# Kernel tuning notes

Hardware: AMD Instinct MI355X
Metric: run time of the kernel (lower is better)

Reference implementation:

```python
import jax, jax.numpy as jnp
import numpy as np

N, F, E, A, H = 50000, 64, 1600000, 8, 16
RECEPTIVE_FIELD = 7


def setup_inputs() -> dict:
    key = jax.random.key(0)
    ks = jax.random.split(key, 12)
    inp = {
        "x": jax.random.normal(ks[0], (N, F), dtype=jnp.float32),
        "edge_index": jax.random.randint(ks[1], (2, E), 0, N, dtype=jnp.int64),
        "w1": jax.random.normal(ks[2], (F, H), dtype=jnp.float32) * 0.1,
        "b1": jax.random.normal(ks[3], (H,), dtype=jnp.float32) * 0.1,
        "w2": jax.random.normal(ks[4], (H, H), dtype=jnp.float32) * 0.1,
        "b2": jax.random.normal(ks[5], (H,), dtype=jnp.float32) * 0.1,
        "w3": jax.random.normal(ks[6], (H, F), dtype=jnp.float32) * 0.1,
        "b3": jax.random.normal(ks[7], (F,), dtype=jnp.float32) * 0.1,
        "fc1_w": jax.random.normal(ks[8], ((1 + RECEPTIVE_FIELD) * F, F), dtype=jnp.float32) * 0.05,
        "fc1_b": jax.random.normal(ks[9], (F,), dtype=jnp.float32) * 0.05,
        "fc2_w": jax.random.normal(ks[10], (F, A), dtype=jnp.float32) * 0.1,
        "fc2_b": jax.random.normal(ks[11], (A,), dtype=jnp.float32) * 0.1,
    }
    return inp


def _mlp(x, w1, b1, w2, b2, w3, b3):
    h = jax.nn.relu(x @ w1 + b1)
    h = jax.nn.relu(h @ w2 + b2)
    return h @ w3 + b3


def _agg_mean(x, src, dst):
    # scatter-mean: mean of source-node features over incoming edges per target
    s = jax.ops.segment_sum(x[src], dst, num_segments=N)          # [N, F]
    cnt = jax.ops.segment_sum(jnp.ones((src.shape[0], 1), x.dtype), dst, num_segments=N)
    return s / jnp.maximum(cnt, 1.0)  # nodes with no in-edges -> 0 (torch mean aggr)


def reference(x, edge_index, w1, b1, w2, b2, w3, b3, fc1_w, fc1_b, fc2_w, fc2_b):
    src, dst = edge_index[0], edge_index[1]
    mlp = lambda t: _mlp(t, w1, b1, w2, b2, w3, b3)
    fields = [mlp(mlp(x))]
    for i in range(RECEPTIVE_FIELD):
        x_ = mlp(x)
        for _ in range(i + 1):
            x_ = _agg_mean(x_, src, dst)
        fields.append(mlp(x_))
    f = jnp.concatenate(fields, axis=1)          # [N, 8*F]
    h = f @ fc1_w + fc1_b                        # [N, F]
    logits = h @ fc2_w + fc2_b                   # [N, A]
    return jax.nn.softmax(logits, axis=-1)       # Categorical probs
```

## Files before the change

### kernel.cpp

```cpp
#include <hip/hip_runtime.h>


#define NB2MAX 400
#define NBLK   256
#define CAP2   32
#define CAPC   48
#define CAPB   6144
#define OVCAP  1024
#define LCAP   6144
#define CAPN   64

__global__ __launch_bounds__(1024) void binfill_k(
    const int* __restrict__ src, const int* __restrict__ dst, int E, int n,
    int* __restrict__ gcur, int* __restrict__ ovbuf,
    int* __restrict__ bins, int* __restrict__ cnts,
    const float* __restrict__ w1, const float* __restrict__ w3,
    const float* __restrict__ b3, const float* __restrict__ fc1w,
    const float* __restrict__ fc1b, const float* __restrict__ fc2w,
    const float* __restrict__ fc2b,
    float* __restrict__ M, float* __restrict__ cvec,
    float* __restrict__ W31, float* __restrict__ c31) {
    __shared__ int lbuf[NB2MAX * CAP2];
    __shared__ int lcnt[NB2MAX];
    __shared__ int lflush[NB2MAX];
    int tid = threadIdx.x;
    int NB = (n + 127) >> 7;

    if ((int)blockIdx.x >= NBLK) {
        float* fl = (float*)lbuf;
        int s = (int)blockIdx.x - NBLK;
        if (s == 0) {
            if (tid < 256) {
                int i = tid >> 4, j = tid & 15;
                float a = 0.f;
                for (int g = 0; g < 64; g++) a += w3[i * 64 + g] * w1[g * 16 + j];
                W31[tid] = a;
            } else if (tid < 272) {
                int j = tid - 256;
                float a = 0.f;
                for (int g = 0; g < 64; g++) a += b3[g] * w1[g * 16 + j];
                c31[j] = a;
            } else if (tid >= 320 && tid < 384) {
                int h = tid - 320;
                float a = 0.f;
                for (int r = 0; r < 512; r++) a += b3[r & 63] * fc1w[r * 64 + h];
                fl[h] = a;
            }
            __syncthreads();
            if (tid < 8) {
                float a = fc2b[tid];
                for (int h = 0; h < 64; h++) a += (fc1b[h] + fl[h]) * fc2w[h * 8 + tid];
                cvec[tid] = a;
            }
        } else {
            int k = s - 1;
            {
                int i = tid >> 6, h = tid & 63;
                float a = 0.f;
                const float* f1 = fc1w + (size_t)(k * 64) * 64 + h;
                for (int g = 0; g < 64; g++) a += w3[i * 64 + g] * f1[g * 64];
                fl[i * 64 + h] = a;
            }
            __syncthreads();
            if (tid < 128) {
                int i = tid >> 3, j = tid & 7;
                float a = 0.f;
                for (int h = 0; h < 64; h++) a += fl[i * 64 + h] * fc2w[h * 8 + j];
                M[k * 128 + i * 8 + j] = a;
            }
        }
        return;
    }

    for (int b = tid; b < NB; b += 1024) { lcnt[b] = 0; lflush[b] = 0; }
    __syncthreads();
    int blk = blockIdx.x;
    int chunk = (E + NBLK - 1) / NBLK;
    int beg = blk * chunk;
    int end = beg + chunk; if (end > E) end = E;
    for (int t0 = beg; t0 < end; t0 += 1024) {
        int e = t0 + tid;
        if (e < end) {
            int d = dst[e], s = src[e];
            if ((unsigned)d < (unsigned)n && (unsigned)s < (unsigned)n) {
                int b = d >> 7;
                int pk = ((d & 127) << 16) | s;
                int pos = atomicAdd(&lcnt[b], 1);
                if (pos < CAP2) lbuf[b * CAP2 + pos] = pk;
                else {
                    int p = atomicAdd(&gcur[b], 1);
                    if (p < OVCAP) ovbuf[b * OVCAP + p] = pk;
                }
            }
        }
        __syncthreads();
        for (int b = tid; b < NB; b += 1024) {
            int cnt = lcnt[b]; if (cnt > CAP2) cnt = CAP2;
            int fl2 = lflush[b];
            size_t cell = ((size_t)b * NBLK + blk) * CAPC;
            int base = 0;
            while (cnt - base >= 16) {
                if (fl2 + 16 <= CAPC) {
                    int* dp = bins + cell + fl2;
                    #pragma unroll
                    for (int q = 0; q < 16; q++) dp[q] = lbuf[b * CAP2 + base + q];
                    fl2 += 16;
                } else {
                    int p = atomicAdd(&gcur[b], 16);
                    for (int q = 0; q < 16; q++)
                        if (p + q < OVCAP) ovbuf[b * OVCAP + p + q] = lbuf[b * CAP2 + base + q];
                }
                base += 16;
            }
            int rem = cnt - base;
            if (base > 0)
                for (int q = 0; q < rem; q++) lbuf[b * CAP2 + q] = lbuf[b * CAP2 + base + q];
            lcnt[b] = rem; lflush[b] = fl2;
        }
        __syncthreads();
    }
    for (int b = tid; b < NB; b += 1024) {
        int cnt = lcnt[b]; if (cnt > CAP2) cnt = CAP2;
        int fl2 = lflush[b];
        size_t cell = ((size_t)b * NBLK + blk) * CAPC;
        if (fl2 + cnt <= CAPC) {
            for (int q = 0; q < cnt; q++) bins[cell + fl2 + q] = lbuf[b * CAP2 + q];
            fl2 += cnt;
        } else {
            int p = atomicAdd(&gcur[b], cnt);
            for (int q = 0; q < cnt; q++)
                if (p + q < OVCAP) ovbuf[b * OVCAP + p + q] = lbuf[b * CAP2 + q];
        }
        cnts[(size_t)blk * NB + b] = fl2;
    }
}

__global__ __launch_bounds__(256) void csr2p_k(
    const int* __restrict__ bins, const int* __restrict__ cnts,
    const int* __restrict__ gcur, const int* __restrict__ ovbuf,
    unsigned short* __restrict__ csrp_s, int2* __restrict__ nd_s,
    int* __restrict__ csr, int2* __restrict__ be, int* __restrict__ lcnt3,
    const float* __restrict__ x, float* __restrict__ z0, float* __restrict__ z1,
    float* __restrict__ logits,
    const float* __restrict__ w1, const float* __restrict__ b1,
    const float* __restrict__ w2, const float* __restrict__ b2,
    const float* __restrict__ W31, const float* __restrict__ c31,
    const float* __restrict__ M0, const float* __restrict__ cvec,
    int n, int NBARG) {
    int tid = threadIdx.x;
    if ((int)blockIdx.x < NBARG) {
        __shared__ int hist[128], pref[128], cur[128], slot[128];
        __shared__ int scnt[NBLK];
        __shared__ int lbuf[LCAP];
        __shared__ int sov;
        __shared__ int ccnt[3], cbase[3];
        int NB = (n + 127) >> 7;
        int b = blockIdx.x;
        if (tid < 128) { hist[tid] = 0; cur[tid] = 0; }
        if (tid < 3) ccnt[tid] = 0;
        scnt[tid] = cnts[(size_t)tid * NB + b];
        if (tid == 0) {
            int g = gcur[b];
            sov = g < 0 ? 0 : (g > OVCAP ? OVCAP : g);
        }
        __syncthreads();
        {
            int c = scnt[tid];
            size_t cell = ((size_t)b * NBLK + tid) * CAPC;
            for (int i = 0; i < c; i++) atomicAdd(&hist[bins[cell + i] >> 16], 1);
        }
        if (tid == 0)
            for (int i = 0; i < sov; i++) atomicAdd(&hist[ovbuf[b * OVCAP + i] >> 16], 1);
        __syncthreads();
        if (tid == 0) {
            int r = 0;
            for (int i = 0; i < 128; i++) { pref[i] = r; r += hist[i]; }
        }
        __syncthreads();
        {
            int c = scnt[tid];
            size_t cell = ((size_t)b * NBLK + tid) * CAPC;
            for (int i = 0; i < c; i++) {
                int pk = bins[cell + i];
                int dl = pk >> 16;
                int pos = pref[dl] + atomicAdd(&cur[dl], 1);
                if (pos < LCAP) lbuf[pos] = pk & 0xffff;
            }
        }
        if (tid == 0) {
            for (int i = 0; i < sov; i++) {
                int pk = ovbuf[b * OVCAP + i];
                int dl = pk >> 16;
                int pos = pref[dl] + atomicAdd(&cur[dl], 1);
                if (pos < LCAP) lbuf[pos] = pk & 0xffff;
            }
        }
        __syncthreads();
        int myc = -1, lpos = 0;
        if (tid < 128) {
            int d = (b << 7) + tid;
            if (d < n) {
                int cnt = hist[tid];
                myc = cnt <= 32 ? 0 : (cnt <= 48 ? 1 : 2);
                lpos = atomicAdd(&ccnt[myc], 1);
            }
        }
        __syncthreads();
        if (tid < 3) cbase[tid] = atomicAdd(&lcnt3[tid], ccnt[tid]);
        __syncthreads();
        if (myc >= 0) {
            int d = (b << 7) + tid;
            int cnt = hist[tid];
            int s = myc * n + cbase[myc] + lpos;
            slot[tid] = s;
            nd_s[s] = make_int2(d, cnt);
            if (cnt > CAPN) {
                int s0 = b * CAPB + pref[tid];
                be[d] = make_int2(s0 + CAPN, s0 + cnt);
                for (int j = CAPN; j < cnt; j++)
                    csr[s0 + j] = lbuf[pref[tid] + j] << 2;
            }
        }
        __syncthreads();
        for (int q = tid; q < 128 * CAPN; q += 256) {
            int dl = q >> 6, j = q & 63;
            int d = (b << 7) + dl;
            if (d >= n) break;
            int cnt = hist[dl];
            int v = (j < cnt) ? lbuf[pref[dl] + j] : n;
            int pos = ((j & 3) << 4) | (j >> 2);
            csrp_s[(size_t)slot[dl] * CAPN + pos] = (unsigned short)v;
        }
        return;
    }
    __shared__ float sw1[1024], sw2[256], sW[256], sM[128];
    __shared__ float sb1[16], sb2[16], sc[16], scv[8];
    for (int i = tid; i < 1024; i += 256) sw1[i] = w1[i];
    sw2[tid] = w2[tid & 255];
    sW[tid & 255] = W31[tid & 255];
    if (tid < 128) sM[tid] = M0[tid];
    if (tid < 16) { sb1[tid] = b1[tid]; sb2[tid] = b2[tid]; sc[tid] = c31[tid]; }
    if (tid < 8) scv[tid] = cvec[tid];
    __syncthreads();
    if ((int)blockIdx.x == NBARG && tid < 16) {
        z0[(size_t)n * 16 + tid] = 0.f;
        z1[(size_t)n * 16 + tid] = 0.f;
    }
    int nid = ((int)blockIdx.x - NBARG) * 256 + tid;
    if (nid >= n) return;
    float t1[16];
    #pragma unroll
    for (int j = 0; j < 16; j++) t1[j] = sb1[j];
    const float4* xp = (const float4*)(x + (size_t)nid * 64);
    #pragma unroll
    for (int q = 0; q < 16; q++) {
        float4 v = xp[q];
        #pragma unroll
        for (int j = 0; j < 16; j++)
            t1[j] += v.x * sw1[(4 * q) * 16 + j] + v.y * sw1[(4 * q + 1) * 16 + j]
                   + v.z * sw1[(4 * q + 2) * 16 + j] + v.w * sw1[(4 * q + 3) * 16 + j];
    }
    #pragma unroll
    for (int j = 0; j < 16; j++) t1[j] = fmaxf(t1[j], 0.f);
    float t2[16];
    #pragma unroll
    for (int j = 0; j < 16; j++) {
        float a = sb2[j];
        #pragma unroll
        for (int i = 0; i < 16; i++) a += t1[i] * sw2[i * 16 + j];
        t2[j] = fmaxf(a, 0.f);
    }
    float z[16];
    #pragma unroll
    for (int j = 0; j < 16; j++) {
        float a = sc[j];
        #pragma unroll
        for (int i = 0; i < 16; i++) a += t2[i] * sW[i * 16 + j];
        z[j] = a;
    }
    float4* zo = (float4*)(z0 + (size_t)nid * 16);
    #pragma unroll
    for (int q = 0; q < 4; q++)
        zo[q] = make_float4(z[4 * q], z[4 * q + 1], z[4 * q + 2], z[4 * q + 3]);
    float h[16], f2[16];
    #pragma unroll
    for (int i = 0; i < 16; i++) h[i] = fmaxf(z[i] + sb1[i], 0.f);
    #pragma unroll
    for (int j = 0; j < 16; j++) {
        float a = sb2[j];
        #pragma unroll
        for (int i = 0; i < 16; i++) a += h[i] * sw2[i * 16 + j];
        f2[j] = fmaxf(a, 0.f);
    }
    float* lp = logits + (size_t)nid * 8;
    #pragma unroll
    for (int j = 0; j < 8; j++) {
        float l = scv[j];
        #pragma unroll
        for (int i = 0; i < 16; i++) l += f2[i] * sM[i * 8 + j];
        lp[j] = l;
    }
}

__global__ __launch_bounds__(256, 4) void hop_k(
    const float* __restrict__ zin, float* __restrict__ zout, float* __restrict__ logits,
    const unsigned short* __restrict__ csrp_s, const int2* __restrict__ nd_s,
    const int2* __restrict__ be, const int* __restrict__ csr,
    const int* __restrict__ lcnt3,
    const float* __restrict__ w2, const float* __restrict__ b1,
    const float* __restrict__ b2, const float* __restrict__ M, int n, int FB) {
    __shared__ float sw2[256], sM[128], sb1[16], sb2[16];
    int tid = threadIdx.x;
    if ((int)blockIdx.x < FB) {
        sw2[tid] = w2[tid];
        if (tid < 128) sM[tid] = M[tid];
        if (tid < 16) { sb1[tid] = b1[tid]; sb2[tid] = b2[tid]; }
        __syncthreads();
        int nid = blockIdx.x * 256 + tid;
        if (nid >= n) return;
        float h[16];
        const float4* zp = (const float4*)(zin + (size_t)nid * 16);
        #pragma unroll
        for (int q = 0; q < 4; q++) {
            float4 v = zp[q];
            h[4 * q] = v.x; h[4 * q + 1] = v.y; h[4 * q + 2] = v.z; h[4 * q + 3] = v.w;
        }
        #pragma unroll
        for (int i = 0; i < 16; i++) h[i] = fmaxf(h[i] + sb1[i], 0.f);
        float t2[16];
        #pragma unroll
        for (int j = 0; j < 16; j++) {
            float a = sb2[j];
            #pragma unroll
            for (int i = 0; i < 16; i++) a += h[i] * sw2[i * 16 + j];
            t2[j] = fmaxf(a, 0.f);
        }
        float* lp = logits + (size_t)nid * 8;
        #pragma unroll
        for (int j = 0; j < 8; j++) {
            float l = 0.f;
            #pragma unroll
            for (int i = 0; i < 16; i++) l += t2[i] * sM[i * 8 + j];
            lp[j] += l;
        }
        return;
    }
    int wave = tid >> 6;
    int lane = tid & 63;
    int quarter = lane >> 4;
    int l16 = lane & 15;
    int t4 = l16 >> 2, ch = l16 & 3;
    int idx = (((int)blockIdx.x - FB) * 4 + wave) * 4 + quarter;
    if (idx >= n) return;
    int ns = lcnt3[0], nm = lcnt3[1];
    int tier; size_t row;
    if (idx < ns)           { tier = 0; row = (size_t)idx; }
    else if (idx < ns + nm) { tier = 1; row = (size_t)n + (idx - ns); }
    else                    { tier = 2; row = 2 * (size_t)n + (idx - ns - nm); }
    int2 nd = nd_s[row];
    int node = nd.x, degi = nd.y;
    const uint4* ip = (const uint4*)(csrp_s + (row << 6));
    uint4 pa = ip[t4 * 2];
    int r0 = pa.x & 0xffff, r1 = pa.x >> 16;
    int r2 = pa.y & 0xffff, r3 = pa.y >> 16;
    int r4 = pa.z & 0xffff, r5 = pa.z >> 16;
    int r6 = pa.w & 0xffff, r7 = pa.w >> 16;
    const float4* z4 = (const float4*)zin;
    float4 v0 = z4[((size_t)r0 << 2) + ch];
    float4 v1 = z4[((size_t)r1 << 2) + ch];
    float4 v2 = z4[((size_t)r2 << 2) + ch];
    float4 v3 = z4[((size_t)r3 << 2) + ch];
    float4 v4 = z4[((size_t)r4 << 2) + ch];
    float4 v5 = z4[((size_t)r5 << 2) + ch];
    float4 v6 = z4[((size_t)r6 << 2) + ch];
    float4 v7 = z4[((size_t)r7 << 2) + ch];
    float ax = ((v0.x + v1.x) + (v2.x + v3.x)) + ((v4.x + v5.x) + (v6.x + v7.x));
    float ay = ((v0.y + v1.y) + (v2.y + v3.y)) + ((v4.y + v5.y) + (v6.y + v7.y));
    float az = ((v0.z + v1.z) + (v2.z + v3.z)) + ((v4.z + v5.z) + (v6.z + v7.z));
    float aw = ((v0.w + v1.w) + (v2.w + v3.w)) + ((v4.w + v5.w) + (v6.w + v7.w));
    if (tier >= 1) {
        uint4 pb = ip[t4 * 2 + 1];
        int r8 = pb.x & 0xffff, r9 = pb.x >> 16;
        int rA = pb.y & 0xffff, rB = pb.y >> 16;
        float4 v8 = z4[((size_t)r8 << 2) + ch];
        float4 v9 = z4[((size_t)r9 << 2) + ch];
        float4 vA = z4[((size_t)rA << 2) + ch];
        float4 vB = z4[((size_t)rB << 2) + ch];
        ax += (v8.x + v9.x) + (vA.x + vB.x);
        ay += (v8.y + v9.y) + (vA.y + vB.y);
        az += (v8.z + v9.z) + (vA.z + vB.z);
        aw += (v8.w + v9.w) + (vA.w + vB.w);
        if (tier == 2) {
            int rC = pb.z & 0xffff, rD = pb.z >> 16;
            int rE = pb.w & 0xffff, rF = pb.w >> 16;
            float4 vC = z4[((size_t)rC << 2) + ch];
            float4 vD = z4[((size_t)rD << 2) + ch];
            float4 vE = z4[((size_t)rE << 2) + ch];
            float4 vF = z4[((size_t)rF << 2) + ch];
            ax += (vC.x + vD.x) + (vE.x + vF.x);
            ay += (vC.y + vD.y) + (vE.y + vF.y);
            az += (vC.z + vD.z) + (vE.z + vF.z);
            aw += (vC.w + vD.w) + (vE.w + vF.w);
            if (degi > CAPN) {
                int2 r = be[node];
                for (int q = r.x + t4; q < r.y; q += 4) {
                    float4 v = z4[(size_t)csr[q] + ch];
                    ax += v.x; ay += v.y; az += v.z; aw += v.w;
                }
            }
        }
    }
    #pragma unroll
    for (int off = 8; off >= 4; off >>= 1) {
        ax += __shfl_down(ax, off, 16);
        ay += __shfl_down(ay, off, 16);
        az += __shfl_down(az, off, 16);
        aw += __shfl_down(aw, off, 16);
    }
    if (l16 < 4) {
        float inv = 1.f / (float)(degi > 0 ? degi : 1);
        ((float4*)(zout + (size_t)node * 16))[l16] =
            make_float4(ax * inv, ay * inv, az * inv, aw * inv);
    }
}

__global__ __launch_bounds__(256) void fieldsoft_k(
    const float* __restrict__ z, float* __restrict__ logits,
    const float* __restrict__ w2, const float* __restrict__ b1,
    const float* __restrict__ b2, const float* __restrict__ M, int n) {
    __shared__ float sw2[256], sM[128], sb1[16], sb2[16];
    int tid = threadIdx.x;
    sw2[tid] = w2[tid];
    if (tid < 128) sM[tid] = M[tid];
    if (tid < 16) { sb1[tid] = b1[tid]; sb2[tid] = b2[tid]; }
    __syncthreads();
    int nid = blockIdx.x * 256 + tid;
    if (nid >= n) return;
    float h[16];
    const float4* zp = (const float4*)(z + (size_t)nid * 16);
    #pragma unroll
    for (int q = 0; q < 4; q++) {
        float4 v = zp[q];
        h[4 * q] = v.x; h[4 * q + 1] = v.y; h[4 * q + 2] = v.z; h[4 * q + 3] = v.w;
    }
    #pragma unroll
    for (int i = 0; i < 16; i++) h[i] = fmaxf(h[i] + sb1[i], 0.f);
    float t2[16];
    #pragma unroll
    for (int j = 0; j < 16; j++) {
        float a = sb2[j];
        #pragma unroll
        for (int i = 0; i < 16; i++) a += h[i] * sw2[i * 16 + j];
        t2[j] = fmaxf(a, 0.f);
    }
    float4* lp4 = (float4*)(logits + (size_t)nid * 8);
    float4 l0 = lp4[0], l1 = lp4[1];
    float v[8] = {l0.x, l0.y, l0.z, l0.w, l1.x, l1.y, l1.z, l1.w};
    #pragma unroll
    for (int j = 0; j < 8; j++) {
        float l = 0.f;
        #pragma unroll
        for (int i = 0; i < 16; i++) l += t2[i] * sM[i * 8 + j];
        v[j] += l;
    }
    float m = v[0];
    #pragma unroll
    for (int j = 1; j < 8; j++) m = fmaxf(m, v[j]);
    float s = 0.f;
    #pragma unroll
    for (int j = 0; j < 8; j++) { v[j] = expf(v[j] - m); s += v[j]; }
    float inv = 1.f / s;
    lp4[0] = make_float4(v[0] * inv, v[1] * inv, v[2] * inv, v[3] * inv);
    lp4[1] = make_float4(v[4] * inv, v[5] * inv, v[6] * inv, v[7] * inv);
}

extern "C" void kernel_launch(void* const* d_in, const int* in_sizes, int n_in,
                              void* d_out, int out_size, void* d_ws, size_t ws_size,
                              hipStream_t stream) {
    const float* x    = (const float*)d_in[0];
    const int*   ei   = (const int*)d_in[1];
    const float* w1   = (const float*)d_in[2];
    const float* b1   = (const float*)d_in[3];
    const float* w2   = (const float*)d_in[4];
    const float* b2   = (const float*)d_in[5];
    const float* w3   = (const float*)d_in[6];
    const float* b3   = (const float*)d_in[7];
    const float* fc1w = (const float*)d_in[8];
    const float* fc1b = (const float*)d_in[9];
    const float* fc2w = (const float*)d_in[10];
    const float* fc2b = (const float*)d_in[11];
    float* out = (float*)d_out;

    int n = in_sizes[0] / 64;
    int E = in_sizes[1] / 2;
    int NB = (n + 127) >> 7;
    const int* src = ei;
    const int* dst = ei + E;

    char* ws = (char*)d_ws;
    auto carve = [&](size_t bytes) {
        char* p = ws;
        ws += (bytes + 255) & ~((size_t)255);
        return p;
    };
    int*   gcur    = (int*)carve((size_t)NB * 4);
    int*   lcnt3   = (int*)carve(16);
    int*   ovbuf   = (int*)carve((size_t)NB * OVCAP * 4);
    int*   binsbuf = (int*)carve((size_t)NB * NBLK * CAPC * 4);
    int*   cnts    = (int*)carve((size_t)NBLK * NB * 4);
    unsigned short* csrp_s = (unsigned short*)carve((size_t)3 * n * CAPN * 2);
    int2*  nd_s    = (int2*)carve((size_t)3 * n * 8);
    int*   csr     = (int*)carve((size_t)NB * CAPB * 4);
    int2*  be      = (int2*)carve((size_t)n * 8);
    float* buf0    = (float*)carve((size_t)(n + 1) * 16 * 4);
    float* buf1    = (float*)carve((size_t)(n + 1) * 16 * 4);
    float* M       = (float*)carve(1024 * 4);
    float* cvec    = (float*)carve(8 * 4);
    float* W31     = (float*)carve(256 * 4);
    float* c31     = (float*)carve(16 * 4);

    size_t gpad = ((size_t)NB * 4 + 255) & ~((size_t)255);
    hipMemsetAsync(gcur, 0, gpad + 16, stream);
    binfill_k<<<NBLK + 9, 1024, 0, stream>>>(src, dst, E, n, gcur, ovbuf, binsbuf, cnts,
                                             w1, w3, b3, fc1w, fc1b, fc2w, fc2b,
                                             M, cvec, W31, c31);

    int FB = (n + 255) / 256;
    int AB = (n + 15) / 16;
    csr2p_k<<<NB + FB, 256, 0, stream>>>(binsbuf, cnts, gcur, ovbuf,
                                         csrp_s, nd_s, csr, be, lcnt3,
                                         x, buf0, buf1, out, w1, b1, w2, b2,
                                         W31, c31, M, cvec, n, NB);

    float* cur = buf0;
    float* nxt = buf1;
    hop_k<<<AB, 256, 0, stream>>>(cur, nxt, out, csrp_s, nd_s, be, csr, lcnt3,
                                  w2, b1, b2, M, n, 0);
    { float* t = cur; cur = nxt; nxt = t; }
    for (int k = 1; k <= 6; k++) {
        hop_k<<<FB + AB, 256, 0, stream>>>(cur, nxt, out, csrp_s, nd_s, be, csr,
                                           lcnt3, w2, b1, b2, M + k * 128, n, FB);
        float* t = cur; cur = nxt; nxt = t;
    }
    fieldsoft_k<<<FB, 256, 0, stream>>>(cur, out, w2, b1, b2, M + 7 * 128, n);
}
```

Before: 260.8 us.

## Store hop features in fp16 and split CSR build from projection kernel

```diff
diff --git a/kernel.cpp b/kernel.cpp
--- a/kernel.cpp
+++ b/kernel.cpp
@@ -1,4 +1,5 @@
 #include <hip/hip_runtime.h>
+#include <hip/hip_fp16.h>
 
 
 #define NB2MAX 400
@@ -135,106 +136,115 @@
     }
 }
 
-__global__ __launch_bounds__(256) void csr2p_k(
+__global__ __launch_bounds__(256) void csr2_k(
     const int* __restrict__ bins, const int* __restrict__ cnts,
     const int* __restrict__ gcur, const int* __restrict__ ovbuf,
     unsigned short* __restrict__ csrp_s, int2* __restrict__ nd_s,
     int* __restrict__ csr, int2* __restrict__ be, int* __restrict__ lcnt3,
-    const float* __restrict__ x, float* __restrict__ z0, float* __restrict__ z1,
+    int n) {
+    __shared__ int hist[128], pref[128], cur[128], slot[128];
+    __shared__ int scnt[NBLK];
+    __shared__ int lbuf[LCAP];
+    __shared__ int sov;
+    __shared__ int ccnt[3], cbase[3];
+    int tid = threadIdx.x;
+    int NB = (n + 127) >> 7;
+    int b = blockIdx.x;
+    if (tid < 128) { hist[tid] = 0; cur[tid] = 0; }
+    if (tid < 3) ccnt[tid] = 0;
+    scnt[tid] = cnts[(size_t)tid * NB + b];
+    if (tid == 0) {
+        int g = gcur[b];
+        sov = g < 0 ? 0 : (g > OVCAP ? OVCAP : g);
+    }
+    __syncthreads();
+    {
+        int c = scnt[tid];
+        size_t cell = ((size_t)b * NBLK + tid) * CAPC;
+        for (int i = 0; i < c; i++) atomicAdd(&hist[bins[cell + i] >> 16], 1);
+    }
+    if (tid == 0)
+        for (int i = 0; i < sov; i++) atomicAdd(&hist[ovbuf[b * OVCAP + i] >> 16], 1);
+    __syncthreads();
+    if (tid == 0) {
+        int r = 0;
+        for (int i = 0; i < 128; i++) { pref[i] = r; r += hist[i]; }
+    }
+    __syncthreads();
+    {
+        int c = scnt[tid];
+        size_t cell = ((size_t)b * NBLK + tid) * CAPC;
+        for (int i = 0; i < c; i++) {
+            int pk = bins[cell + i];
+            int dl = pk >> 16;
+            int pos = pref[dl] + atomicAdd(&cur[dl], 1);
+            if (pos < LCAP) lbuf[pos] = pk & 0xffff;
+        }
+    }
+    if (tid == 0) {
+        for (int i = 0; i < sov; i++) {
+            int pk = ovbuf[b * OVCAP + i];
+            int dl = pk >> 16;
+            int pos = pref[dl] + atomicAdd(&cur[dl], 1);
+            if (pos < LCAP) lbuf[pos] = pk & 0xffff;
+        }
+    }
+    __syncthreads();
+    int myc = -1, lpos = 0;
+    if (tid < 128) {
+        int d = (b << 7) + tid;
+        if (d < n) {
+            int cnt = hist[tid];
+            myc = cnt <= 32 ? 0 : (cnt <= 48 ? 1 : 2);
+            lpos = atomicAdd(&ccnt[myc], 1);
+        }
+    }
+    __syncthreads();
+    if (tid < 3) cbase[tid] = atomicAdd(&lcnt3[tid], ccnt[tid]);
+    __syncthreads();
+    if (myc >= 0) {
+        int d = (b << 7) + tid;
+        int cnt = hist[tid];
+        int s = myc * n + cbase[myc] + lpos;
+        slot[tid] = s;
+        nd_s[s] = make_int2(d, cnt);
+        if (cnt > CAPN) {
+            int s0 = b * CAPB + pref[tid];
+            be[d] = make_int2(s0 + CAPN, s0 + cnt);
+            for (int j = CAPN; j < cnt; j++)
+                csr[s0 + j] = lbuf[pref[tid] + j] << 2;
+        }
+    }
+    __syncthreads();
+    for (int q = tid; q < 128 * CAPN; q += 256) {
+        int dl = q >> 6, j = q & 63;
+        int d = (b << 7) + dl;
+        if (d >= n) break;
+        int cnt = hist[dl];
+        int v = (j < cnt) ? lbuf[pref[dl] + j] : n;
+        int pos = ((j & 3) << 4) | (j >> 2);
+        csrp_s[(size_t)slot[dl] * CAPN + pos] = (unsigned short)v;
+    }
+}
+
+__device__ __forceinline__ void acc_row(uint2 u, float& ax, float& ay,
+                                        float& az, float& aw) {
+    __half2 p = *reinterpret_cast<const __half2*>(&u.x);
+    __half2 q = *reinterpret_cast<const __half2*>(&u.y);
+    float2 f = __half22float2(p), g = __half22float2(q);
+    ax += f.x; ay += f.y; az += g.x; aw += g.y;
+}
+
+__global__ __launch_bounds__(256) void proj_k(
+    const float* __restrict__ x, __half* __restrict__ z0, __half* __restrict__ z1,
     float* __restrict__ logits,
     const float* __restrict__ w1, const float* __restrict__ b1,
     const float* __restrict__ w2, const float* __restrict__ b2,
     const float* __restrict__ W31, const float* __restrict__ c31,
-    const float* __restrict__ M0, const float* __restrict__ cvec,
-    int n, int NBARG) {
-    int tid = threadIdx.x;
-    if ((int)blockIdx.x < NBARG) {
-        __shared__ int hist[128], pref[128], cur[128], slot[128];
-        __shared__ int scnt[NBLK];
-        __shared__ int lbuf[LCAP];
-        __shared__ int sov;
-        __shared__ int ccnt[3], cbase[3];
-        int NB = (n + 127) >> 7;
-        int b = blockIdx.x;
-        if (tid < 128) { hist[tid] = 0; cur[tid] = 0; }
-        if (tid < 3) ccnt[tid] = 0;
-        scnt[tid] = cnts[(size_t)tid * NB + b];
-        if (tid == 0) {
-            int g = gcur[b];
-            sov = g < 0 ? 0 : (g > OVCAP ? OVCAP : g);
-        }
-        __syncthreads();
-        {
-            int c = scnt[tid];
-            size_t cell = ((size_t)b * NBLK + tid) * CAPC;
-            for (int i = 0; i < c; i++) atomicAdd(&hist[bins[cell + i] >> 16], 1);
-        }
-        if (tid == 0)
-            for (int i = 0; i < sov; i++) atomicAdd(&hist[ovbuf[b * OVCAP + i] >> 16], 1);
-        __syncthreads();
-        if (tid == 0) {
-            int r = 0;
-            for (int i = 0; i < 128; i++) { pref[i] = r; r += hist[i]; }
-        }
-        __syncthreads();
-        {
-            int c = scnt[tid];
-            size_t cell = ((size_t)b * NBLK + tid) * CAPC;
-            for (int i = 0; i < c; i++) {
-                int pk = bins[cell + i];
-                int dl = pk >> 16;
-                int pos = pref[dl] + atomicAdd(&cur[dl], 1);
-                if (pos < LCAP) lbuf[pos] = pk & 0xffff;
-            }
-        }
-        if (tid == 0) {
-            for (int i = 0; i < sov; i++) {
-                int pk = ovbuf[b * OVCAP + i];
-                int dl = pk >> 16;
-                int pos = pref[dl] + atomicAdd(&cur[dl], 1);
-                if (pos < LCAP) lbuf[pos] = pk & 0xffff;
-            }
-        }
-        __syncthreads();
-        int myc = -1, lpos = 0;
-        if (tid < 128) {
-            int d = (b << 7) + tid;
-            if (d < n) {
-                int cnt = hist[tid];
-                myc = cnt <= 32 ? 0 : (cnt <= 48 ? 1 : 2);
-                lpos = atomicAdd(&ccnt[myc], 1);
-            }
-        }
-        __syncthreads();
-        if (tid < 3) cbase[tid] = atomicAdd(&lcnt3[tid], ccnt[tid]);
-        __syncthreads();
-        if (myc >= 0) {
-            int d = (b << 7) + tid;
-            int cnt = hist[tid];
-            int s = myc * n + cbase[myc] + lpos;
-            slot[tid] = s;
-            nd_s[s] = make_int2(d, cnt);
-            if (cnt > CAPN) {
-                int s0 = b * CAPB + pref[tid];
-                be[d] = make_int2(s0 + CAPN, s0 + cnt);
-                for (int j = CAPN; j < cnt; j++)
-                    csr[s0 + j] = lbuf[pref[tid] + j] << 2;
-            }
-        }
-        __syncthreads();
-        for (int q = tid; q < 128 * CAPN; q += 256) {
-            int dl = q >> 6, j = q & 63;
-            int d = (b << 7) + dl;
-            if (d >= n) break;
-            int cnt = hist[dl];
-            int v = (j < cnt) ? lbuf[pref[dl] + j] : n;
-            int pos = ((j & 3) << 4) | (j >> 2);
-            csrp_s[(size_t)slot[dl] * CAPN + pos] = (unsigned short)v;
-        }
-        return;
-    }
+    const float* __restrict__ M0, const float* __restrict__ cvec, int n) {
     __shared__ float sw1[1024], sw2[256], sW[256], sM[128];
     __shared__ float sb1[16], sb2[16], sc[16], scv[8];
+    int tid = threadIdx.x;
     for (int i = tid; i < 1024; i += 256) sw1[i] = w1[i];
     sw2[tid] = w2[tid & 255];
     sW[tid & 255] = W31[tid & 255];
@@ -242,11 +252,11 @@
     if (tid < 16) { sb1[tid] = b1[tid]; sb2[tid] = b2[tid]; sc[tid] = c31[tid]; }
     if (tid < 8) scv[tid] = cvec[tid];
     __syncthreads();
-    if ((int)blockIdx.x == NBARG && tid < 16) {
-        z0[(size_t)n * 16 + tid] = 0.f;
-        z1[(size_t)n * 16 + tid] = 0.f;
-    }
-    int nid = ((int)blockIdx.x - NBARG) * 256 + tid;
+    if (blockIdx.x == 0 && tid < 16) {
+        ((unsigned short*)z0)[(size_t)n * 16 + tid] = 0;
+        ((unsigned short*)z1)[(size_t)n * 16 + tid] = 0;
+    }
+    int nid = blockIdx.x * 256 + tid;
     if (nid >= n) return;
     float t1[16];
     #pragma unroll
@@ -278,10 +288,10 @@
         for (int i = 0; i < 16; i++) a += t2[i] * sW[i * 16 + j];
         z[j] = a;
     }
-    float4* zo = (float4*)(z0 + (size_t)nid * 16);
-    #pragma unroll
-    for (int q = 0; q < 4; q++)
-        zo[q] = make_float4(z[4 * q], z[4 * q + 1], z[4 * q + 2], z[4 * q + 3]);
+    __half2* zo = (__half2*)(z0 + (size_t)nid * 16);
+    #pragma unroll
+    for (int q = 0; q < 8; q++)
+        zo[q] = __floats2half2_rn(z[2 * q], z[2 * q + 1]);
     float h[16], f2[16];
     #pragma unroll
     for (int i = 0; i < 16; i++) h[i] = fmaxf(z[i] + sb1[i], 0.f);
@@ -303,7 +313,8 @@
 }
 
 __global__ __launch_bounds__(256, 4) void hop_k(
-    const float* __restrict__ zin, float* __restrict__ zout, float* __restrict__ logits,
+    const __half* __restrict__ zin, __half* __restrict__ zout,
+    float* __restrict__ logits,
     const unsigned short* __restrict__ csrp_s, const int2* __restrict__ nd_s,
     const int2* __restrict__ be, const int* __restrict__ csr,
     const int* __restrict__ lcnt3,
@@ -319,11 +330,11 @@
         int nid = blockIdx.x * 256 + tid;
         if (nid >= n) return;
         float h[16];
-        const float4* zp = (const float4*)(zin + (size_t)nid * 16);
-        #pragma unroll
-        for (int q = 0; q < 4; q++) {
-            float4 v = zp[q];
-            h[4 * q] = v.x; h[4 * q + 1] = v.y; h[4 * q + 2] = v.z; h[4 * q + 3] = v.w;
+        const __half2* zp = (const __half2*)(zin + (size_t)nid * 16);
+        #pragma unroll
+        for (int q = 0; q < 8; q++) {
+            float2 f = __half22float2(zp[q]);
+            h[2 * q] = f.x; h[2 * q + 1] = f.y;
         }
         #pragma unroll
         for (int i = 0; i < 16; i++) h[i] = fmaxf(h[i] + sb1[i], 0.f);
@@ -365,47 +376,44 @@
     int r2 = pa.y & 0xffff, r3 = pa.y >> 16;
     int r4 = pa.z & 0xffff, r5 = pa.z >> 16;
     int r6 = pa.w & 0xffff, r7 = pa.w >> 16;
-    const float4* z4 = (const float4*)zin;
-    float4 v0 = z4[((size_t)r0 << 2) + ch];
-    float4 v1 = z4[((size_t)r1 << 2) + ch];
-    float4 v2 = z4[((size_t)r2 << 2) + ch];
-    float4 v3 = z4[((size_t)r3 << 2) + ch];
-    float4 v4 = z4[((size_t)r4 << 2) + ch];
-    float4 v5 = z4[((size_t)r5 << 2) + ch];
-    float4 v6 = z4[((size_t)r6 << 2) + ch];
-    float4 v7 = z4[((size_t)r7 << 2) + ch];
-    float ax = ((v0.x + v1.x) + (v2.x + v3.x)) + ((v4.x + v5.x) + (v6.x + v7.x));
-    float ay = ((v0.y + v1.y) + (v2.y + v3.y)) + ((v4.y + v5.y) + (v6.y + v7.y));
-    float az = ((v0.z + v1.z) + (v2.z + v3.z)) + ((v4.z + v5.z) + (v6.z + v7.z));
-    float aw = ((v0.w + v1.w) + (v2.w + v3.w)) + ((v4.w + v5.w) + (v6.w + v7.w));
+    const uint2* z2 = (const uint2*)zin;
+    uint2 u0 = z2[((size_t)r0 << 2) + ch];
+    uint2 u1 = z2[((size_t)r1 << 2) + ch];
+    uint2 u2 = z2[((size_t)r2 << 2) + ch];
+    uint2 u3 = z2[((size_t)r3 << 2) + ch];
+    uint2 u4 = z2[((size_t)r4 << 2) + ch];
+    uint2 u5 = z2[((size_t)r5 << 2) + ch];
+    uint2 u6 = z2[((size_t)r6 << 2) + ch];
+    uint2 u7 = z2[((size_t)r7 << 2) + ch];
+    float ax = 0.f, ay = 0.f, az = 0.f, aw = 0.f;
+    acc_row(u0, ax, ay, az, aw); acc_row(u1, ax, ay, az, aw);
+    acc_row(u2, ax, ay, az, aw); acc_row(u3, ax, ay, az, aw);
+    acc_row(u4, ax, ay, az, aw); acc_row(u5, ax, ay, az, aw);
+    acc_row(u6, ax, ay, az, aw); acc_row(u7, ax, ay, az, aw);
     if (tier >= 1) {
         uint4 pb = ip[t4 * 2 + 1];
         int r8 = pb.x & 0xffff, r9 = pb.x >> 16;
         int rA = pb.y & 0xffff, rB = pb.y >> 16;
-        float4 v8 = z4[((size_t)r8 << 2) + ch];
-        float4 v9 = z4[((size_t)r9 << 2) + ch];
-        float4 vA = z4[((size_t)rA << 2) + ch];
-        float4 vB = z4[((size_t)rB << 2) + ch];
-        ax += (v8.x + v9.x) + (vA.x + vB.x);
-        ay += (v8.y + v9.y) + (vA.y + vB.y);
-        az += (v8.z + v9.z) + (vA.z + vB.z);
-        aw += (v8.w + v9.w) + (vA.w + vB.w);
+        uint2 u8 = z2[((size_t)r8 << 2) + ch];
+        uint2 u9 = z2[((size_t)r9 << 2) + ch];
+        uint2 uA = z2[((size_t)rA << 2) + ch];
+        uint2 uB = z2[((size_t)rB << 2) + ch];
+        acc_row(u8, ax, ay, az, aw); acc_row(u9, ax, ay, az, aw);
+        acc_row(uA, ax, ay, az, aw); acc_row(uB, ax, ay, az, aw);
         if (tier == 2) {
             int rC = pb.z & 0xffff, rD = pb.z >> 16;
             int rE = pb.w & 0xffff, rF = pb.w >> 16;
-            float4 vC = z4[((size_t)rC << 2) + ch];
-            float4 vD = z4[((size_t)rD << 2) + ch];
-            float4 vE = z4[((size_t)rE << 2) + ch];
-            float4 vF = z4[((size_t)rF << 2) + ch];
-            ax += (vC.x + vD.x) + (vE.x + vF.x);
-            ay += (vC.y + vD.y) + (vE.y + vF.y);
-            az += (vC.z + vD.z) + (vE.z + vF.z);
-            aw += (vC.w + vD.w) + (vE.w + vF.w);
+            uint2 uC = z2[((size_t)rC << 2) + ch];
+            uint2 uD = z2[((size_t)rD << 2) + ch];
+            uint2 uE = z2[((size_t)rE << 2) + ch];
+            uint2 uF = z2[((size_t)rF << 2) + ch];
+            acc_row(uC, ax, ay, az, aw); acc_row(uD, ax, ay, az, aw);
+            acc_row(uE, ax, ay, az, aw); acc_row(uF, ax, ay, az, aw);
             if (degi > CAPN) {
                 int2 r = be[node];
                 for (int q = r.x + t4; q < r.y; q += 4) {
-                    float4 v = z4[(size_t)csr[q] + ch];
-                    ax += v.x; ay += v.y; az += v.z; aw += v.w;
+                    uint2 u = z2[(size_t)csr[q] + ch];
+                    acc_row(u, ax, ay, az, aw);
                 }
             }
         }
@@ -419,13 +427,17 @@
     }
     if (l16 < 4) {
         float inv = 1.f / (float)(degi > 0 ? degi : 1);
-        ((float4*)(zout + (size_t)node * 16))[l16] =
-            make_float4(ax * inv, ay * inv, az * inv, aw * inv);
+        __half2 h01 = __floats2half2_rn(ax * inv, ay * inv);
+        __half2 h23 = __floats2half2_rn(az * inv, aw * inv);
+        uint2 w;
+        w.x = *reinterpret_cast<unsigned int*>(&h01);
+        w.y = *reinterpret_cast<unsigned int*>(&h23);
+        ((uint2*)(zout + (size_t)node * 16))[l16] = w;
     }
 }
 
 __global__ __launch_bounds__(256) void fieldsoft_k(
-    const float* __restrict__ z, float* __restrict__ logits,
+    const __half* __restrict__ z, float* __restrict__ logits,
     const float* __restrict__ w2, const float* __restrict__ b1,
     const float* __restrict__ b2, const float* __restrict__ M, int n) {
     __shared__ float sw2[256], sM[128], sb1[16], sb2[16];
@@ -437,11 +449,11 @@
     int nid = blockIdx.x * 256 + tid;
     if (nid >= n) return;
     float h[16];
-    const float4* zp = (const float4*)(z + (size_t)nid * 16);
-    #pragma unroll
-    for (int q = 0; q < 4; q++) {
-        float4 v = zp[q];
-        h[4 * q] = v.x; h[4 * q + 1] = v.y; h[4 * q + 2] = v.z; h[4 * q + 3] = v.w;
+    const __half2* zp = (const __half2*)(z + (size_t)nid * 16);
+    #pragma unroll
+    for (int q = 0; q < 8; q++) {
+        float2 f = __half22float2(zp[q]);
+        h[2 * q] = f.x; h[2 * q + 1] = f.y;
     }
     #pragma unroll
     for (int i = 0; i < 16; i++) h[i] = fmaxf(h[i] + sb1[i], 0.f);
@@ -512,8 +524,8 @@
     int2*  nd_s    = (int2*)carve((size_t)3 * n * 8);
     int*   csr     = (int*)carve((size_t)NB * CAPB * 4);
     int2*  be      = (int2*)carve((size_t)n * 8);
-    float* buf0    = (float*)carve((size_t)(n + 1) * 16 * 4);
-    float* buf1    = (float*)carve((size_t)(n + 1) * 16 * 4);
+    __half* buf0   = (__half*)carve((size_t)(n + 1) * 16 * 2);
+    __half* buf1   = (__half*)carve((size_t)(n + 1) * 16 * 2);
     float* M       = (float*)carve(1024 * 4);
     float* cvec    = (float*)carve(8 * 4);
     float* W31     = (float*)carve(256 * 4);
@@ -524,23 +536,23 @@
     binfill_k<<<NBLK + 9, 1024, 0, stream>>>(src, dst, E, n, gcur, ovbuf, binsbuf, cnts,
                                              w1, w3, b3, fc1w, fc1b, fc2w, fc2b,
                                              M, cvec, W31, c31);
+    csr2_k<<<NB, 256, 0, stream>>>(binsbuf, cnts, gcur, ovbuf,
+                                   csrp_s, nd_s, csr, be, lcnt3, n);
 
     int FB = (n + 255) / 256;
     int AB = (n + 15) / 16;
-    csr2p_k<<<NB + FB, 256, 0, stream>>>(binsbuf, cnts, gcur, ovbuf,
-                                         csrp_s, nd_s, csr, be, lcnt3,
-                                         x, buf0, buf1, out, w1, b1, w2, b2,
-                                         W31, c31, M, cvec, n, NB);
-
-    float* cur = buf0;
-    float* nxt = buf1;
+    proj_k<<<FB, 256, 0, stream>>>(x, buf0, buf1, out, w1, b1, w2, b2,
+                                   W31, c31, M, cvec, n);
+
+    __half* cur = buf0;
+    __half* nxt = buf1;
     hop_k<<<AB, 256, 0, stream>>>(cur, nxt, out, csrp_s, nd_s, be, csr, lcnt3,
                                   w2, b1, b2, M, n, 0);
-    { float* t = cur; cur = nxt; nxt = t; }
+    { __half* t = cur; cur = nxt; nxt = t; }
     for (int k = 1; k <= 6; k++) {
         hop_k<<<FB + AB, 256, 0, stream>>>(cur, nxt, out, csrp_s, nd_s, be, csr,
                                            lcnt3, w2, b1, b2, M + k * 128, n, FB);
-        float* t = cur; cur = nxt; nxt = t;
+        __half* t = cur; cur = nxt; nxt = t;
     }
     fieldsoft_k<<<FB, 256, 0, stream>>>(cur, out, w2, b1, b2, M + 7 * 128, n);
 }
```

New measurement: 240.2 us. -7.9%, faster.
